# Kernel tuning notes

Hardware: AMD Instinct MI355X
Metric: run time of the kernel (lower is better)

The kernel has to match this reference:

```python
import jax, jax.numpy as jnp
import numpy as np
from jax import lax

VS = VT = 32000; E = 512; H = 512; B = 32; S = 64; T = 48; D = 10
PAD_ID = 0


def setup_inputs() -> dict:
    key = jax.random.key(0)
    ks = jax.random.split(key, 24)
    g = lambda k, shp: (jax.random.normal(k, shp, jnp.float32) * 0.05)
    inp = {
        'source': jax.random.randint(ks[0], (S, B), 1, VS).astype(jnp.int32),
        'target': jax.random.randint(ks[1], (T, B), 1, VT).astype(jnp.int32),
        'encode_len': jnp.full((B,), S, dtype=jnp.int32),
        'src_emb': g(ks[2], (VS, E)),
        'tar_emb': g(ks[3], (VT, E)),
        'enc_Wih0': g(ks[4], (4 * H, E)),   'enc_Whh0': g(ks[5], (4 * H, H)), 'enc_b0': g(ks[6], (4 * H,)),
        'enc_Wih1': g(ks[7], (4 * H, H)),   'enc_Whh1': g(ks[8], (4 * H, H)), 'enc_b1': g(ks[9], (4 * H,)),
        'dec_Wih0': g(ks[10], (4 * H, E + H)), 'dec_Whh0': g(ks[11], (4 * H, H)), 'dec_b0': g(ks[12], (4 * H,)),
        'dec_Wih1': g(ks[13], (4 * H, H)),  'dec_Whh1': g(ks[14], (4 * H, H)), 'dec_b1': g(ks[15], (4 * H,)),
        'W_ht2tan': g(ks[16], (H, H)),
        'W_tan2pt': g(ks[17], (1, H)),
        'W_ct2ht': g(ks[18], (H, 2 * H)),
        'W_final': g(ks[19], (VT, H)),
    }
    return inp


def _lstm_cell(x, h, c, Wih, Whh, b):
    z = x @ Wih.T + h @ Whh.T + b          # [B,4H]
    i, f, g, o = jnp.split(z, 4, axis=-1)  # torch gate order i,f,g,o
    i = jax.nn.sigmoid(i); f = jax.nn.sigmoid(f)
    g = jnp.tanh(g);       o = jax.nn.sigmoid(o)
    c2 = f * c + i * g
    return o * jnp.tanh(c2), c2


def _lstm_layer(xs, Wih, Whh, b):
    Bd = xs.shape[1]; Hd = Whh.shape[1]
    h0 = jnp.zeros((Bd, Hd), xs.dtype); c0 = jnp.zeros((Bd, Hd), xs.dtype)
    def step(carry, x):
        h, c = carry
        h2, c2 = _lstm_cell(x, h, c, Wih, Whh, b)
        return (h2, c2), h2
    (hT, cT), ys = lax.scan(step, (h0, c0), xs)
    return ys, hT, cT


def reference(source, target, encode_len, src_emb, tar_emb,
              enc_Wih0, enc_Whh0, enc_b0, enc_Wih1, enc_Whh1, enc_b1,
              dec_Wih0, dec_Whh0, dec_b0, dec_Wih1, dec_Whh1, dec_b1,
              W_ht2tan, W_tan2pt, W_ct2ht, W_final):
    # ---- encode ----
    x = src_emb[source]                                   # [S,B,E]
    h1, hn0, cn0 = _lstm_layer(x, enc_Wih0, enc_Whh0, enc_b0)
    h2, hn1, cn1 = _lstm_layer(h1, enc_Wih1, enc_Whh1, enc_b1)
    encode_h = jnp.transpose(h2, (1, 0, 2))               # [B,S,H]

    # ---- decode with Luong local (windowed) attention ----
    y = tar_emb[target]                                   # [T,B,E]
    pos = jnp.arange(S, dtype=jnp.float32)[None, :]       # [1,S]
    valid = jnp.arange(S)[None, :] < encode_len[:, None]  # [B,S]
    elen_f = encode_len.astype(jnp.float32)
    denom = D * D / 2.0

    def dec_step(carry, y_t):
        h0, c0, h1_, c1_, ht = carry
        xin = jnp.concatenate([y_t, ht], axis=-1)          # [B,E+H]
        h0n, c0n = _lstm_cell(xin, h0, c0, dec_Wih0, dec_Whh0, dec_b0)
        h1n, c1n = _lstm_cell(h0n, h1_, c1_, dec_Wih1, dec_Whh1, dec_b1)
        yt = h1n                                           # [B,H]
        pt = jax.nn.sigmoid(jnp.tanh(yt @ W_ht2tan.T) @ W_tan2pt.T)[:, 0] * elen_f  # [B]
        scores = jnp.einsum('bh,bsh->bs', yt, encode_h)    # [B,S]
        scores = jnp.where(valid, scores, -jnp.inf)
        align = jax.nn.softmax(scores, axis=-1)
        gauss = jnp.exp(-((pos - pt[:, None]) ** 2) / denom)
        at = align * gauss                                 # [B,S]
        ct = jnp.einsum('bs,bsh->bh', at, encode_h)        # [B,H]
        htn = jnp.tanh(jnp.concatenate([ct, yt], axis=-1) @ W_ct2ht.T)
        return (h0n, c0n, h1n, c1n, htn), htn

    ht0 = jnp.zeros((B, H), jnp.float32)
    _, decode_out = lax.scan(dec_step, (hn0, cn0, hn1, cn1, ht0), y)  # [T,B,H]

    logits = decode_out @ W_final.T                        # [T,B,V]
    P = jax.nn.log_softmax(logits, axis=-1)
    tar_mask = (target != PAD_ID).astype(jnp.float32)      # [T,B]
    lp = jnp.take_along_axis(P[:-1], target[1:, :, None].astype(jnp.int32), axis=-1)[..., 0]
    lp = lp * tar_mask[1:]
    return lp.sum(axis=0)                                  # [B]
```

## Files before the change

kernel.cpp:

```cpp
#include <hip/hip_runtime.h>
#include <math.h>

#define NB   32
#define HD   512
#define SEQ  64
#define TSEQ 48
#define NCHUNK 250
#define MROWS  1536
#define XSTR 260
#define BARSLOT 32
#define MASTER 255
#define NT   512
#define SCOPE_AG __HIP_MEMORY_SCOPE_AGENT

typedef __bf16 bf16x8 __attribute__((ext_vector_type(8)));
typedef float f32x4 __attribute__((ext_vector_type(4)));

__device__ __forceinline__ float sigmf(float x) { return 1.0f / (1.0f + expf(-x)); }

__device__ __forceinline__ float ldc_f32(const float* p) {
  return __hip_atomic_load((float*)p, __ATOMIC_RELAXED, SCOPE_AG);
}
__device__ __forceinline__ void stc_f32(float* p, float v) {
  __hip_atomic_store(p, v, __ATOMIC_RELAXED, SCOPE_AG);
}
__device__ __forceinline__ unsigned long long ldc_u64(const float* p) {
  return __hip_atomic_load((unsigned long long*)p, __ATOMIC_RELAXED, SCOPE_AG);
}

__global__ __launch_bounds__(256) void zero_kernel(float* p, int n) {
  int i = blockIdx.x * 256 + threadIdx.x;
  if (i < n) p[i] = 0.0f;
}

__device__ __forceinline__ void gbar(int* bars, int& stg) {
  int* arrv = bars;
  int* rel = bars + 256 * BARSLOT;
  __syncthreads();
  ++stg;
  if (threadIdx.x == 0) {
    asm volatile("s_waitcnt vmcnt(0)" ::: "memory");
    __hip_atomic_store(arrv + blockIdx.x * BARSLOT, stg, __ATOMIC_RELAXED, SCOPE_AG);
  }
  if (blockIdx.x == MASTER) {
    if (threadIdx.x < 256) {
      while (__hip_atomic_load(arrv + threadIdx.x * BARSLOT, __ATOMIC_RELAXED, SCOPE_AG) < stg)
        __builtin_amdgcn_s_sleep(1);
    }
    __syncthreads();
    if (threadIdx.x == 0)
      __hip_atomic_store(rel, stg, __ATOMIC_RELAXED, SCOPE_AG);
  } else {
    if (threadIdx.x == 0) {
      while (__hip_atomic_load(rel, __ATOMIC_RELAXED, SCOPE_AG) < stg)
        __builtin_amdgcn_s_sleep(1);
    }
  }
  __syncthreads();
}

#define CSEL_X(J)  ((J) < 2 ? x1 : ((J) < 4 ? x2 : x3))
#define CSEL_I(J)  ((J) < 2 ? i1 : ((J) < 4 ? i2 : i3))
#define CSEL_W(J)  ((J) < 2 ? W1 : ((J) < 4 ? W2 : W3))
#define CSEL_LD(J) ((J) < 2 ? ld1 : ((J) < 4 ? ld2 : ld3))
#define CSEL_CO(J) ((J) < 2 ? co1 : ((J) < 4 ? co2 : co3))

#define CLOADJ(J) do {                                                        \
    const float* Xj = CSEL_X(J); const int* Ij = CSEL_I(J);                   \
    const int xo = ((J) & 1) * 256;                                           \
    _Pragma("unroll")                                                         \
    for (int it = 0; it < 4; ++it) {                                          \
      const int idx = tid + it * NT; const int bb = idx >> 6, f4 = idx & 63;  \
      if (Ij) {                                                               \
        rg[it] = *(const float4*)(Xj + (size_t)Ij[bb] * HD + xo + f4 * 4);    \
      } else {                                                                \
        const float* s_ = Xj + (size_t)bb * HD + xo + f4 * 4;                 \
        ((unsigned long long*)&rg[it])[0] = ldc_u64(s_);                      \
        ((unsigned long long*)&rg[it])[1] = ldc_u64(s_ + 2);                  \
      }                                                                       \
    } } while (0)

#define CSTJ(BUF) do {                                                        \
    _Pragma("unroll")                                                         \
    for (int it = 0; it < 4; ++it) {                                          \
      const int idx = tid + it * NT; const int bb = idx >> 6, f4 = idx & 63;  \
      *(float4*)&(BUF)[bb * XSTR + f4 * 4] = rg[it];                          \
    } } while (0)

#define CCOMP(J, BUF) do {                                                    \
    const float* W_ = CSEL_W(J); const int ld_ = CSEL_LD(J);                  \
    const int co_ = CSEL_CO(J) + ((J) & 1) * 256;                             \
    const float* xr = (BUF) + b * XSTR + ks * CQ;                             \
    const float* wq = W_ + co_ + ks * CQ;                                     \
    const float* w0 = wq + (size_t)(hi) * ld_;                                \
    const float* w1 = wq + (size_t)(512 + hi) * ld_;                          \
    const float* w2 = wq + (size_t)(1024 + hi) * ld_;                         \
    const float* w3 = wq + (size_t)(1536 + hi) * ld_;                         \
    _Pragma("unroll 4")                                                       \
    for (int k = 0; k < CQ; k += 4) {                                         \
      const float4 xv = *(const float4*)(xr + k);                             \
      const float4 wa = *(const float4*)(w0 + k);                             \
      const float4 wb2 = *(const float4*)(w1 + k);                            \
      const float4 wc = *(const float4*)(w2 + k);                             \
      const float4 wd = *(const float4*)(w3 + k);                             \
      a0 += xv.x*wa.x + xv.y*wa.y + xv.z*wa.z + xv.w*wa.w;                    \
      a1 += xv.x*wb2.x + xv.y*wb2.y + xv.z*wb2.z + xv.w*wb2.w;                \
      a2 += xv.x*wc.x + xv.y*wc.y + xv.z*wc.z + xv.w*wc.w;                    \
      a3 += xv.x*wd.x + xv.y*wd.y + xv.z*wd.z + xv.w*wd.w;                    \
    } } while (0)

template<int HPB, int KS, bool HAS3>
__device__ __forceinline__ void cell_stage(int blk,
    const float* x1, const int* i1, const float* W1, int ld1, int co1,
    const float* x2, const int* i2, const float* W2, int ld2, int co2,
    const float* x3, const int* i3, const float* W3, int ld3, int co3,
    const float* bias, float* cbuf, float* hout, float* hseq, float* LDSf) {
  const int tid = threadIdx.x;
  const int b = tid & 31;
  const int q = tid >> 5;
  const int hl = q & (HPB - 1);
  const int ks = q / HPB;
  const int CQ = 256 / KS;
  const int hi = blk * HPB + hl;
  float* bufA = LDSf;
  float* bufB = LDSf + 32 * XSTR;
  float* zp = LDSf + 2 * 32 * XSTR;
  float a0 = 0.f, a1 = 0.f, a2 = 0.f, a3 = 0.f;
  float4 rg[4];
  CLOADJ(0); CSTJ(bufA);
  __syncthreads();
  CLOADJ(1); CCOMP(0, bufA); CSTJ(bufB); __syncthreads();
  CLOADJ(2); CCOMP(1, bufB); CSTJ(bufA); __syncthreads();
  CLOADJ(3); CCOMP(2, bufA); CSTJ(bufB); __syncthreads();
  if constexpr (HAS3) {
    CLOADJ(4); CCOMP(3, bufB); CSTJ(bufA); __syncthreads();
    CLOADJ(5); CCOMP(4, bufA); CSTJ(bufB); __syncthreads();
    CCOMP(5, bufB);
  } else {
    CCOMP(3, bufB);
  }
  zp[((hl * 4 + 0) * KS + ks) * 33 + b] = a0;
  zp[((hl * 4 + 1) * KS + ks) * 33 + b] = a1;
  zp[((hl * 4 + 2) * KS + ks) * 33 + b] = a2;
  zp[((hl * 4 + 3) * KS + ks) * 33 + b] = a3;
  __syncthreads();
  if (tid < 32 * HPB) {
    const int b2 = tid & 31, h2 = tid >> 5;
    const int hi2 = blk * HPB + h2;
    float z[4];
    #pragma unroll
    for (int g = 0; g < 4; ++g) {
      float s = bias[g * 512 + hi2];
      #pragma unroll
      for (int k2 = 0; k2 < KS; ++k2) s += zp[((h2 * 4 + g) * KS + k2) * 33 + b2];
      z[g] = s;
    }
    const float ig = sigmf(z[0]), fg = sigmf(z[1]);
    const float gg = tanhf(z[2]), og = sigmf(z[3]);
    const int off = b2 * HD + hi2;
    const float c2 = fg * ldc_f32(cbuf + off) + ig * gg;
    const float hv = og * tanhf(c2);
    stc_f32(cbuf + off, c2);
    stc_f32(hout + off, hv);
    if (hseq) stc_f32(hseq + off, hv);
  }
}

#define GLOADJ(J) do {                                                        \
    const float* Xj = ((J) < 2 ? x1 : x2); const int xo = ((J) & 1) * 256;    \
    _Pragma("unroll")                                                         \
    for (int it = 0; it < 4; ++it) {                                          \
      const int idx = tid + it * NT; const int bb = idx >> 6, f4 = idx & 63;  \
      const float* s_ = Xj + (size_t)bb * HD + xo + f4 * 4;                   \
      ((unsigned long long*)&rg[it])[0] = ldc_u64(s_);                        \
      ((unsigned long long*)&rg[it])[1] = ldc_u64(s_ + 2);                    \
    } } while (0)

#define GCOMP(J, BUF) do {                                                    \
    const float* W_ = ((J) < 2 ? W1 : W2);                                    \
    const int ld_ = ((J) < 2 ? ld1 : ld2);                                    \
    const int co_ = ((J) < 2 ? co1 : co2) + ((J) & 1) * 256;                  \
    const float* xr = (BUF) + b * XSTR + ks * CQ;                             \
    const float* wp = W_ + (size_t)r * ld_ + co_ + ks * CQ;                   \
    _Pragma("unroll 4")                                                       \
    for (int k = 0; k < CQ; k += 4) {                                         \
      const float4 xv = *(const float4*)(xr + k);                             \
      const float4 wv = *(const float4*)(wp + k);                             \
      acc += xv.x*wv.x + xv.y*wv.y + xv.z*wv.z + xv.w*wv.w;                   \
    } } while (0)

template<int RPB, int KS, bool HAS2>
__device__ __forceinline__ void gemv_stage(int blk,
    const float* x1, const float* W1, int ld1, int co1,
    const float* x2, const float* W2, int ld2, int co2,
    float* out1, float* out2, float* LDSf) {
  const int tid = threadIdx.x;
  const int b = tid & 31;
  const int q = tid >> 5;
  const int rl = q & (RPB - 1);
  const int ks = q / RPB;
  const int CQ = 256 / KS;
  const int r = blk * RPB + rl;
  float* bufA = LDSf;
  float* bufB = LDSf + 32 * XSTR;
  float* zp = LDSf + 2 * 32 * XSTR;
  float acc = 0.f;
  float4 rg[4];
  GLOADJ(0); CSTJ(bufA);
  __syncthreads();
  GLOADJ(1); GCOMP(0, bufA); CSTJ(bufB); __syncthreads();
  if constexpr (HAS2) {
    GLOADJ(2); GCOMP(1, bufB); CSTJ(bufA); __syncthreads();
    GLOADJ(3); GCOMP(2, bufA); CSTJ(bufB); __syncthreads();
    GCOMP(3, bufB);
  } else {
    GCOMP(1, bufB);
  }
  zp[(rl * KS + ks) * 33 + b] = acc;
  __syncthreads();
  if (tid < 32 * RPB) {
    const int b2 = tid & 31, rl2 = tid >> 5;
    const int r2 = blk * RPB + rl2;
    float s = 0.f;
    #pragma unroll
    for (int k2 = 0; k2 < KS; ++k2) s += zp[(rl2 * KS + k2) * 33 + b2];
    const float tv = tanhf(s);
    stc_f32(out1 + b2 * HD + r2, tv);
    if (out2) stc_f32(out2 + b2 * HD + r2, tv);
  }
}

__device__ void scores_stage(int b, const float* yt, const float* H2,
                             float* scs_g, float* LDSf) {
  const int tid = threadIdx.x;
  float* yts = LDSf;
  float* red = LDSf + 512;
  yts[tid] = ldc_f32(yt + (size_t)b * HD + tid);
  __syncthreads();
  const int s = tid >> 3, part = tid & 7;
  const float* hrow = H2 + (size_t)s * (NB * HD) + (size_t)b * HD + part * 64;
  const float* xr = yts + part * 64;
  float a = 0.f;
  #pragma unroll 8
  for (int k = 0; k < 64; ++k) a += xr[k] * hrow[k];
  red[tid] = a;
  __syncthreads();
  if (tid < 64) {
    float v = 0.f;
    #pragma unroll
    for (int p = 0; p < 8; ++p) v += red[tid * 8 + p];
    stc_f32(scs_g + b * 64 + tid, v);
  }
}

__device__ void attn_stage(int b, const float* tanW, const float* w2pt,
    const float* H2, const int* elen, const float* scs_g, float* ct,
    float* LDSf) {
  const int tid = threadIdx.x;
  float* red = LDSf;
  float* ats = LDSf + 512;
  float* sc  = LDSf + 580;
  red[tid] = ldc_f32(tanW + (size_t)b * HD + tid) * w2pt[tid];
  __syncthreads();
  #pragma unroll
  for (int s2 = 256; s2 > 0; s2 >>= 1) {
    if (tid < s2) red[tid] += red[tid + s2];
    __syncthreads();
  }
  if (tid == 0) sc[0] = sigmf(red[0]) * (float)elen[b];
  __syncthreads();
  const int L = elen[b];
  const float pt = sc[0];
  if (tid < 64) {
    float v = ldc_f32(scs_g + b * 64 + tid);
    v = (tid < L) ? v : -3.0e38f;
    float mx = v;
    #pragma unroll
    for (int d = 1; d < 64; d <<= 1) mx = fmaxf(mx, __shfl_xor(mx, d));
    float e = (tid < L) ? expf(v - mx) : 0.f;
    float sm = e;
    #pragma unroll
    for (int d = 1; d < 64; d <<= 1) sm += __shfl_xor(sm, d);
    const float al = e / sm;
    const float dd = (float)tid - pt;
    ats[tid] = al * expf(-(dd * dd) * (1.0f / 50.0f));
  }
  __syncthreads();
  {
    const int h = tid;
    float acc = 0.f;
    #pragma unroll 8
    for (int s = 0; s < 64; ++s)
      acc += ats[s] * H2[(size_t)s * (NB * HD) + (size_t)b * HD + h];
    stc_f32(ct + b * HD + h, acc);
  }
}

struct CoopArgs {
  const int *source, *target, *elen;
  const float *src_emb, *tar_emb;
  const float *eW0, *eU0, *eb0, *eW1, *eU1, *eb1;
  const float *dW0, *dU0, *db0, *dW1, *dU1, *db1;
  const float *Wht2tan, *Wtan2pt, *Wct2ht;
  float *c0, *c1, *h0a, *h0b, *h1a, *h1b, *dht, *tanW, *ct, *scs_g, *H1, *H2, *dout;
  int *bars;
};

__global__ __launch_bounds__(NT) void coop_kernel(CoopArgs P) {
  __shared__ float LDSf[2 * 32 * XSTR + 2200];
  const int blk = blockIdx.x;
  int stg = 0;
  float* h0buf[2] = {P.h0a, P.h0b};
  float* h1buf[2] = {P.h1a, P.h1b};
  int p0 = 0, p1 = 0;
  for (int t = 0; t <= SEQ; ++t) {
    if (blk < 128) {
      if (t < SEQ)
        cell_stage<4, 4, false>(blk,
            h0buf[p0], nullptr, P.eU0, 512, 0,
            P.src_emb, P.source + t * NB, P.eW0, 512, 0,
            nullptr, nullptr, nullptr, 0, 0,
            P.eb0, P.c0, h0buf[p0 ^ 1], P.H1 + (size_t)t * NB * HD, LDSf);
    } else {
      if (t >= 1)
        cell_stage<4, 4, false>(blk - 128,
            h1buf[p1], nullptr, P.eU1, 512, 0,
            P.H1 + (size_t)(t - 1) * NB * HD, nullptr, P.eW1, 512, 0,
            nullptr, nullptr, nullptr, 0, 0,
            P.eb1, P.c1, h1buf[p1 ^ 1], P.H2 + (size_t)(t - 1) * NB * HD, LDSf);
    }
    gbar(P.bars, stg);
    if (t < SEQ) p0 ^= 1;
    if (t >= 1) p1 ^= 1;
  }
  for (int t = 0; t < TSEQ; ++t) {
    cell_stage<2, 8, true>(blk,
        h0buf[p0], nullptr, P.dU0, 512, 0,
        P.tar_emb, P.target + t * NB, P.dW0, 1024, 0,
        P.dht, nullptr, P.dW0, 1024, 512,
        P.db0, P.c0, h0buf[p0 ^ 1], nullptr, LDSf);
    gbar(P.bars, stg);
    cell_stage<2, 8, false>(blk,
        h1buf[p1], nullptr, P.dU1, 512, 0,
        h0buf[p0 ^ 1], nullptr, P.dW1, 512, 0,
        nullptr, nullptr, nullptr, 0, 0,
        P.db1, P.c1, h1buf[p1 ^ 1], nullptr, LDSf);
    gbar(P.bars, stg);
    if (blk < 128)
      gemv_stage<4, 4, false>(blk, h1buf[p1 ^ 1], P.Wht2tan, 512, 0,
                              nullptr, nullptr, 0, 0, P.tanW, nullptr, LDSf);
    else if (blk < 160)
      scores_stage(blk - 128, h1buf[p1 ^ 1], P.H2, P.scs_g, LDSf);
    gbar(P.bars, stg);
    if (blk < 32)
      attn_stage(blk, P.tanW, P.Wtan2pt, P.H2, P.elen, P.scs_g, P.ct, LDSf);
    gbar(P.bars, stg);
    gemv_stage<2, 8, true>(blk,
        P.ct, P.Wct2ht, 1024, 0,
        h1buf[p1 ^ 1], P.Wct2ht, 1024, 512,
        P.dht, P.dout + (size_t)t * NB * HD, LDSf);
    gbar(P.bars, stg);
    p0 ^= 1; p1 ^= 1;
  }
}

__device__ __forceinline__ ushort f2bf(float f) {
  unsigned u = __float_as_uint(f);
  u += 0x7fffu + ((u >> 16) & 1u);
  return (ushort)(u >> 16);
}
__global__ __launch_bounds__(256) void cvt_kernel(
    const float* __restrict__ a, ushort* __restrict__ da, int na,
    const float* __restrict__ w, ushort* __restrict__ dw, int nw) {
  int i = (blockIdx.x * 256 + threadIdx.x) * 4;
  if (i < na) {
    float4 v = *(const float4*)(a + i);
    ushort4 o; o.x = f2bf(v.x); o.y = f2bf(v.y); o.z = f2bf(v.z); o.w = f2bf(v.w);
    *(ushort4*)(da + i) = o;
  } else {
    int j = i - na;
    if (j < nw) {
      float4 v = *(const float4*)(w + j);
      ushort4 o; o.x = f2bf(v.x); o.y = f2bf(v.y); o.z = f2bf(v.z); o.w = f2bf(v.w);
      *(ushort4*)(dw + j) = o;
    }
  }
}

__global__ __launch_bounds__(256) void final_gemm_bf(
    const ushort* __restrict__ Au, const ushort* __restrict__ Wu,
    const int* __restrict__ target,
    float* __restrict__ pm, float* __restrict__ pl, float* __restrict__ tlg) {
  const __bf16* A = (const __bf16*)Au;
  const __bf16* W = (const __bf16*)Wu;
  const int tid = threadIdx.x;
  const int wv = tid >> 6, lane = tid & 63;
  const int l15 = lane & 15, quad = lane >> 4;
  const int m0 = blockIdx.y * 64;
  const int nb = blockIdx.x * 128;
  const int n0 = nb + wv * 32;
  const f32x4 zf = {0.f, 0.f, 0.f, 0.f};
  f32x4 acc[4][2];
  #pragma unroll
  for (int mt = 0; mt < 4; ++mt) { acc[mt][0] = zf; acc[mt][1] = zf; }
  const __bf16* ap  = A + (size_t)(m0 + l15) * HD + quad * 8;
  const __bf16* bp0 = W + (size_t)(n0 + l15) * HD + quad * 8;
  const __bf16* bp1 = W + (size_t)(n0 + 16 + l15) * HD + quad * 8;
  #pragma unroll 2
  for (int k0 = 0; k0 < HD; k0 += 32) {
    const bf16x8 b0 = *(const bf16x8*)(bp0 + k0);
    const bf16x8 b1 = *(const bf16x8*)(bp1 + k0);
    #pragma unroll
    for (int mt = 0; mt < 4; ++mt) {
      const bf16x8 av = *(const bf16x8*)(ap + (size_t)mt * 16 * HD + k0);
      acc[mt][0] = __builtin_amdgcn_mfma_f32_16x16x32_bf16(av, b0, acc[mt][0], 0, 0, 0);
      acc[mt][1] = __builtin_amdgcn_mfma_f32_16x16x32_bf16(av, b1, acc[mt][1], 0, 0, 0);
    }
  }
  __shared__ float red[64][5];
  __shared__ float rowm[64];
  #pragma unroll
  for (int mt = 0; mt < 4; ++mt)
    #pragma unroll
    for (int r = 0; r < 4; ++r) {
      float v = fmaxf(acc[mt][0][r], acc[mt][1][r]);
      #pragma unroll
      for (int d = 1; d < 16; d <<= 1) v = fmaxf(v, __shfl_xor(v, d));
      if (l15 == 0) red[mt * 16 + quad * 4 + r][wv] = v;
    }
  __syncthreads();
  if (tid < 64)
    rowm[tid] = fmaxf(fmaxf(red[tid][0], red[tid][1]),
                      fmaxf(red[tid][2], red[tid][3]));
  __syncthreads();
  #pragma unroll
  for (int mt = 0; mt < 4; ++mt)
    #pragma unroll
    for (int r = 0; r < 4; ++r) {
      const float mm = rowm[mt * 16 + quad * 4 + r];
      float s = expf(acc[mt][0][r] - mm) + expf(acc[mt][1][r] - mm);
      #pragma unroll
      for (int d = 1; d < 16; d <<= 1) s += __shfl_xor(s, d);
      if (l15 == 0) red[mt * 16 + quad * 4 + r][wv] = s;
    }
  __syncthreads();
  if (tid < 64) {
    const int row = m0 + tid;
    pm[(size_t)blockIdx.x * MROWS + row] = rowm[tid];
    pl[(size_t)blockIdx.x * MROWS + row] =
        red[tid][0] + red[tid][1] + red[tid][2] + red[tid][3];
  }
  #pragma unroll
  for (int mt = 0; mt < 4; ++mt) {
    const int row = m0 + mt * 16 + quad * 4;
    #pragma unroll
    for (int r = 0; r < 4; ++r) {
      const int t = (row + r) >> 5, bb = (row + r) & 31;
      if (t < TSEQ - 1) {
        const int tg = target[(t + 1) * NB + bb];
        if (n0 + l15 == tg)      tlg[row + r] = acc[mt][0][r];
        if (n0 + 16 + l15 == tg) tlg[row + r] = acc[mt][1][r];
      }
    }
  }
}

__global__ __launch_bounds__(64) void final_reduce(
    const float* __restrict__ pm, const float* __restrict__ pl,
    const float* __restrict__ tlg, const int* __restrict__ target,
    float* __restrict__ out) {
  const int b = blockIdx.x, tid = threadIdx.x;
  float lp = 0.f;
  if (tid < TSEQ - 1) {
    const int row = tid * NB + b;
    float mx = -3.0e38f;
    for (int i = 0; i < NCHUNK; ++i) mx = fmaxf(mx, pm[(size_t)i * MROWS + row]);
    float l = 0.f;
    for (int i = 0; i < NCHUNK; ++i)
      l += pl[(size_t)i * MROWS + row] * expf(pm[(size_t)i * MROWS + row] - mx);
    const float lse = mx + logf(l);
    const float msk = (target[(tid + 1) * NB + b] != 0) ? 1.f : 0.f;
    lp = (tlg[row] - lse) * msk;
  }
  #pragma unroll
  for (int off = 32; off > 0; off >>= 1) lp += __shfl_down(lp, off);
  if (tid == 0) out[b] = lp;
}

extern "C" void kernel_launch(void* const* d_in, const int* in_sizes, int n_in,
                              void* d_out, int out_size, void* d_ws, size_t ws_size,
                              hipStream_t stream) {
  const int* source = (const int*)d_in[0];
  const int* target = (const int*)d_in[1];
  const int* elen   = (const int*)d_in[2];
  const float* src_emb = (const float*)d_in[3];
  const float* tar_emb = (const float*)d_in[4];
  const float* eW0 = (const float*)d_in[5];
  const float* eU0 = (const float*)d_in[6];
  const float* eb0 = (const float*)d_in[7];
  const float* eW1 = (const float*)d_in[8];
  const float* eU1 = (const float*)d_in[9];
  const float* eb1 = (const float*)d_in[10];
  const float* dW0 = (const float*)d_in[11];
  const float* dU0 = (const float*)d_in[12];
  const float* db0 = (const float*)d_in[13];
  const float* dW1 = (const float*)d_in[14];
  const float* dU1 = (const float*)d_in[15];
  const float* db1 = (const float*)d_in[16];
  const float* Wht2tan = (const float*)d_in[17];
  const float* Wtan2pt = (const float*)d_in[18];
  const float* Wct2ht  = (const float*)d_in[19];
  const float* Wfinal  = (const float*)d_in[20];
  float* out = (float*)d_out;

  float* w = (float*)d_ws;
  float* c0  = w; w += NB * HD;
  float* c1  = w; w += NB * HD;
  float* h0a = w; w += NB * HD;
  float* h1a = w; w += NB * HD;
  float* dht = w; w += NB * HD;
  int* bars = (int*)w; w += 257 * BARSLOT;
  float* h0b = w; w += NB * HD;
  float* h1b = w; w += NB * HD;
  float* tanW = w; w += NB * HD;
  float* ct  = w; w += NB * HD;
  float* scs_g = w; w += NB * 64;
  float* H1  = w; w += (size_t)SEQ * NB * HD;
  float* H2  = w; w += (size_t)SEQ * NB * HD;
  float* dout = w; w += (size_t)TSEQ * NB * HD;
  float* pm  = w; w += (size_t)NCHUNK * MROWS;
  float* pl  = w; w += (size_t)NCHUNK * MROWS;
  float* tlg = w; w += MROWS;
  ushort* Abf = (ushort*)w; w += (MROWS * HD) / 2;
  ushort* Wbf = (ushort*)w; w += ((size_t)32000 * HD) / 2;

  const int nzero = 5 * NB * HD + 257 * BARSLOT;
  zero_kernel<<<dim3((nzero + 255) / 256), dim3(256), 0, stream>>>((float*)d_ws, nzero);

  CoopArgs A;
  A.source = source; A.target = target; A.elen = elen;
  A.src_emb = src_emb; A.tar_emb = tar_emb;
  A.eW0 = eW0; A.eU0 = eU0; A.eb0 = eb0;
  A.eW1 = eW1; A.eU1 = eU1; A.eb1 = eb1;
  A.dW0 = dW0; A.dU0 = dU0; A.db0 = db0;
  A.dW1 = dW1; A.dU1 = dU1; A.db1 = db1;
  A.Wht2tan = Wht2tan; A.Wtan2pt = Wtan2pt; A.Wct2ht = Wct2ht;
  A.c0 = c0; A.c1 = c1; A.h0a = h0a; A.h0b = h0b; A.h1a = h1a; A.h1b = h1b;
  A.dht = dht; A.tanW = tanW; A.ct = ct; A.scs_g = scs_g;
  A.H1 = H1; A.H2 = H2; A.dout = dout;
  A.bars = bars;
  void* kargs[] = {&A};
  hipLaunchCooperativeKernel((void*)coop_kernel, dim3(256), dim3(NT), kargs, 0, stream);

  const int na = MROWS * HD;
  const int nw = 32000 * HD;
  const int tot4 = (na + nw) / 4;
  cvt_kernel<<<dim3((tot4 + 255) / 256), dim3(256), 0, stream>>>(
      dout, Abf, na, Wfinal, Wbf, nw);
  final_gemm_bf<<<dim3(NCHUNK, MROWS / 64), dim3(256), 0, stream>>>(
      Abf, Wbf, target, pm, pl, tlg);
  final_reduce<<<dim3(NB), dim3(64), 0, stream>>>(pm, pl, tlg, target, out);

  (void)in_sizes; (void)n_in; (void)out_size; (void)ws_size;
}
```

Baseline: 5.032 ms.

## Use write-once per-step state buffers to allow plain cached loads

Replaces the ping-pong h/dht/tanW/ct/score buffers with arrays that get a fresh slot each timestep, so no address is ever rewritten within the persistent kernel. This lets the reads of recurrent state switch from relaxed atomic agent-scope loads to ordinary vectorized float4 loads, since a stale cached line cannot hold an older value for an address that was never written before. It costs a larger workspace and relies on the L2 coherence and barrier assumptions being sufficient for non-atomic loads across workgroups.

```diff
diff --git a/kernel.cpp b/kernel.cpp
--- a/kernel.cpp
+++ b/kernel.cpp
@@ -24,9 +24,6 @@
 __device__ __forceinline__ void stc_f32(float* p, float v) {
   __hip_atomic_store(p, v, __ATOMIC_RELAXED, SCOPE_AG);
 }
-__device__ __forceinline__ unsigned long long ldc_u64(const float* p) {
-  return __hip_atomic_load((unsigned long long*)p, __ATOMIC_RELAXED, SCOPE_AG);
-}
 
 __global__ __launch_bounds__(256) void zero_kernel(float* p, int n) {
   int i = blockIdx.x * 256 + threadIdx.x;
@@ -59,6 +56,10 @@
   __syncthreads();
 }
 
+__device__ __forceinline__ float* slot(float* z, float* ar, int t) {
+  return t == 0 ? z : ar + (size_t)(t - 1) * (NB * HD);
+}
+
 #define CSEL_X(J)  ((J) < 2 ? x1 : ((J) < 4 ? x2 : x3))
 #define CSEL_I(J)  ((J) < 2 ? i1 : ((J) < 4 ? i2 : i3))
 #define CSEL_W(J)  ((J) < 2 ? W1 : ((J) < 4 ? W2 : W3))
@@ -71,13 +72,9 @@
     _Pragma("unroll")                                                         \
     for (int it = 0; it < 4; ++it) {                                          \
       const int idx = tid + it * NT; const int bb = idx >> 6, f4 = idx & 63;  \
-      if (Ij) {                                                               \
-        rg[it] = *(const float4*)(Xj + (size_t)Ij[bb] * HD + xo + f4 * 4);    \
-      } else {                                                                \
-        const float* s_ = Xj + (size_t)bb * HD + xo + f4 * 4;                 \
-        ((unsigned long long*)&rg[it])[0] = ldc_u64(s_);                      \
-        ((unsigned long long*)&rg[it])[1] = ldc_u64(s_ + 2);                  \
-      }                                                                       \
+      const float* row = Ij ? (Xj + (size_t)Ij[bb] * HD)                      \
+                            : (Xj + (size_t)bb * HD);                         \
+      rg[it] = *(const float4*)(row + xo + f4 * 4);                           \
     } } while (0)
 
 #define CSTJ(BUF) do {                                                        \
@@ -171,9 +168,7 @@
     _Pragma("unroll")                                                         \
     for (int it = 0; it < 4; ++it) {                                          \
       const int idx = tid + it * NT; const int bb = idx >> 6, f4 = idx & 63;  \
-      const float* s_ = Xj + (size_t)bb * HD + xo + f4 * 4;                   \
-      ((unsigned long long*)&rg[it])[0] = ldc_u64(s_);                        \
-      ((unsigned long long*)&rg[it])[1] = ldc_u64(s_ + 2);                    \
+      rg[it] = *(const float4*)(Xj + (size_t)bb * HD + xo + f4 * 4);          \
     } } while (0)
 
 #define GCOMP(J, BUF) do {                                                    \
@@ -235,7 +230,7 @@
   const int tid = threadIdx.x;
   float* yts = LDSf;
   float* red = LDSf + 512;
-  yts[tid] = ldc_f32(yt + (size_t)b * HD + tid);
+  yts[tid] = yt[(size_t)b * HD + tid];
   __syncthreads();
   const int s = tid >> 3, part = tid & 7;
   const float* hrow = H2 + (size_t)s * (NB * HD) + (size_t)b * HD + part * 64;
@@ -260,7 +255,7 @@
   float* red = LDSf;
   float* ats = LDSf + 512;
   float* sc  = LDSf + 580;
-  red[tid] = ldc_f32(tanW + (size_t)b * HD + tid) * w2pt[tid];
+  red[tid] = tanW[(size_t)b * HD + tid] * w2pt[tid];
   __syncthreads();
   #pragma unroll
   for (int s2 = 256; s2 > 0; s2 >>= 1) {
@@ -272,7 +267,7 @@
   const int L = elen[b];
   const float pt = sc[0];
   if (tid < 64) {
-    float v = ldc_f32(scs_g + b * 64 + tid);
+    float v = scs_g[b * 64 + tid];
     v = (tid < L) ? v : -3.0e38f;
     float mx = v;
     #pragma unroll
@@ -302,7 +297,8 @@
   const float *eW0, *eU0, *eb0, *eW1, *eU1, *eb1;
   const float *dW0, *dU0, *db0, *dW1, *dU1, *db1;
   const float *Wht2tan, *Wtan2pt, *Wct2ht;
-  float *c0, *c1, *h0a, *h0b, *h1a, *h1b, *dht, *tanW, *ct, *scs_g, *H1, *H2, *dout;
+  float *c0, *c1, *h0z, *h1z, *dhtz, *h0ar, *h1ar, *dhtar;
+  float *tanWar, *ctar, *scsar, *H1, *H2, *dout;
   int *bars;
 };
 
@@ -310,57 +306,57 @@
   __shared__ float LDSf[2 * 32 * XSTR + 2200];
   const int blk = blockIdx.x;
   int stg = 0;
-  float* h0buf[2] = {P.h0a, P.h0b};
-  float* h1buf[2] = {P.h1a, P.h1b};
-  int p0 = 0, p1 = 0;
   for (int t = 0; t <= SEQ; ++t) {
     if (blk < 128) {
       if (t < SEQ)
         cell_stage<4, 4, false>(blk,
-            h0buf[p0], nullptr, P.eU0, 512, 0,
+            slot(P.h0z, P.h0ar, t), nullptr, P.eU0, 512, 0,
             P.src_emb, P.source + t * NB, P.eW0, 512, 0,
             nullptr, nullptr, nullptr, 0, 0,
-            P.eb0, P.c0, h0buf[p0 ^ 1], P.H1 + (size_t)t * NB * HD, LDSf);
+            P.eb0, P.c0, slot(P.h0z, P.h0ar, t + 1),
+            P.H1 + (size_t)t * NB * HD, LDSf);
     } else {
       if (t >= 1)
         cell_stage<4, 4, false>(blk - 128,
-            h1buf[p1], nullptr, P.eU1, 512, 0,
+            slot(P.h1z, P.h1ar, t - 1), nullptr, P.eU1, 512, 0,
             P.H1 + (size_t)(t - 1) * NB * HD, nullptr, P.eW1, 512, 0,
             nullptr, nullptr, nullptr, 0, 0,
-            P.eb1, P.c1, h1buf[p1 ^ 1], P.H2 + (size_t)(t - 1) * NB * HD, LDSf);
+            P.eb1, P.c1, slot(P.h1z, P.h1ar, t),
+            P.H2 + (size_t)(t - 1) * NB * HD, LDSf);
     }
     gbar(P.bars, stg);
-    if (t < SEQ) p0 ^= 1;
-    if (t >= 1) p1 ^= 1;
   }
   for (int t = 0; t < TSEQ; ++t) {
+    float* h1n = slot(P.h1z, P.h1ar, 65 + t);
     cell_stage<2, 8, true>(blk,
-        h0buf[p0], nullptr, P.dU0, 512, 0,
+        slot(P.h0z, P.h0ar, 64 + t), nullptr, P.dU0, 512, 0,
         P.tar_emb, P.target + t * NB, P.dW0, 1024, 0,
-        P.dht, nullptr, P.dW0, 1024, 512,
-        P.db0, P.c0, h0buf[p0 ^ 1], nullptr, LDSf);
+        slot(P.dhtz, P.dhtar, t), nullptr, P.dW0, 1024, 512,
+        P.db0, P.c0, slot(P.h0z, P.h0ar, 65 + t), nullptr, LDSf);
     gbar(P.bars, stg);
     cell_stage<2, 8, false>(blk,
-        h1buf[p1], nullptr, P.dU1, 512, 0,
-        h0buf[p0 ^ 1], nullptr, P.dW1, 512, 0,
+        slot(P.h1z, P.h1ar, 64 + t), nullptr, P.dU1, 512, 0,
+        slot(P.h0z, P.h0ar, 65 + t), nullptr, P.dW1, 512, 0,
         nullptr, nullptr, nullptr, 0, 0,
-        P.db1, P.c1, h1buf[p1 ^ 1], nullptr, LDSf);
+        P.db1, P.c1, h1n, nullptr, LDSf);
     gbar(P.bars, stg);
     if (blk < 128)
-      gemv_stage<4, 4, false>(blk, h1buf[p1 ^ 1], P.Wht2tan, 512, 0,
-                              nullptr, nullptr, 0, 0, P.tanW, nullptr, LDSf);
+      gemv_stage<4, 4, false>(blk, h1n, P.Wht2tan, 512, 0,
+                              nullptr, nullptr, 0, 0,
+                              P.tanWar + (size_t)t * NB * HD, nullptr, LDSf);
     else if (blk < 160)
-      scores_stage(blk - 128, h1buf[p1 ^ 1], P.H2, P.scs_g, LDSf);
+      scores_stage(blk - 128, h1n, P.H2, P.scsar + (size_t)t * NB * 64, LDSf);
     gbar(P.bars, stg);
     if (blk < 32)
-      attn_stage(blk, P.tanW, P.Wtan2pt, P.H2, P.elen, P.scs_g, P.ct, LDSf);
+      attn_stage(blk, P.tanWar + (size_t)t * NB * HD, P.Wtan2pt, P.H2, P.elen,
+                 P.scsar + (size_t)t * NB * 64,
+                 P.ctar + (size_t)t * NB * HD, LDSf);
     gbar(P.bars, stg);
     gemv_stage<2, 8, true>(blk,
-        P.ct, P.Wct2ht, 1024, 0,
-        h1buf[p1 ^ 1], P.Wct2ht, 1024, 512,
-        P.dht, P.dout + (size_t)t * NB * HD, LDSf);
+        P.ctar + (size_t)t * NB * HD, P.Wct2ht, 1024, 0,
+        h1n, P.Wct2ht, 1024, 512,
+        slot(P.dhtz, P.dhtar, t + 1), P.dout + (size_t)t * NB * HD, LDSf);
     gbar(P.bars, stg);
-    p0 ^= 1; p1 ^= 1;
   }
 }
 
@@ -514,17 +510,18 @@
   float* out = (float*)d_out;
 
   float* w = (float*)d_ws;
-  float* c0  = w; w += NB * HD;
-  float* c1  = w; w += NB * HD;
-  float* h0a = w; w += NB * HD;
-  float* h1a = w; w += NB * HD;
-  float* dht = w; w += NB * HD;
+  float* c0   = w; w += NB * HD;
+  float* c1   = w; w += NB * HD;
+  float* h0z  = w; w += NB * HD;
+  float* h1z  = w; w += NB * HD;
+  float* dhtz = w; w += NB * HD;
   int* bars = (int*)w; w += 257 * BARSLOT;
-  float* h0b = w; w += NB * HD;
-  float* h1b = w; w += NB * HD;
-  float* tanW = w; w += NB * HD;
-  float* ct  = w; w += NB * HD;
-  float* scs_g = w; w += NB * 64;
+  float* h0ar  = w; w += (size_t)112 * NB * HD;
+  float* h1ar  = w; w += (size_t)112 * NB * HD;
+  float* dhtar = w; w += (size_t)48 * NB * HD;
+  float* tanWar = w; w += (size_t)TSEQ * NB * HD;
+  float* ctar   = w; w += (size_t)TSEQ * NB * HD;
+  float* scsar  = w; w += (size_t)TSEQ * NB * 64;
   float* H1  = w; w += (size_t)SEQ * NB * HD;
   float* H2  = w; w += (size_t)SEQ * NB * HD;
   float* dout = w; w += (size_t)TSEQ * NB * HD;
@@ -545,8 +542,10 @@
   A.dW0 = dW0; A.dU0 = dU0; A.db0 = db0;
   A.dW1 = dW1; A.dU1 = dU1; A.db1 = db1;
   A.Wht2tan = Wht2tan; A.Wtan2pt = Wtan2pt; A.Wct2ht = Wct2ht;
-  A.c0 = c0; A.c1 = c1; A.h0a = h0a; A.h0b = h0b; A.h1a = h1a; A.h1b = h1b;
-  A.dht = dht; A.tanW = tanW; A.ct = ct; A.scs_g = scs_g;
+  A.c0 = c0; A.c1 = c1;
+  A.h0z = h0z; A.h1z = h1z; A.dhtz = dhtz;
+  A.h0ar = h0ar; A.h1ar = h1ar; A.dhtar = dhtar;
+  A.tanWar = tanWar; A.ctar = ctar; A.scsar = scsar;
   A.H1 = H1; A.H2 = H2; A.dout = dout;
   A.bars = bars;
   void* kargs[] = {&A};
```

Measured after the change: 5.115 ms. Within noise of the previous version (+1.7%).
